# Kernel optimization log

Hardware: AMD Instinct MI355X
Metric: run time of the kernel (lower is better)

The kernel has to match this reference:

```python
import jax, jax.numpy as jnp
import numpy as np

B, T, N, DIN = 16, 40, 64, 64
H = 256          # n_hid == msg_out == gru_hid (required by the module's own shape constraints)
MSG_HID = 256
DOUT = 64
E = N * (N - 1)  # fully-connected directed graph, no self loops


def _linear_params(key, fin, fout):
    kw, kb = jax.random.split(key)
    s = 1.0 / np.sqrt(fin)
    w = jax.random.uniform(kw, (fout, fin), minval=-s, maxval=s, dtype=jnp.float32)
    b = jax.random.uniform(kb, (fout,), minval=-s, maxval=s, dtype=jnp.float32)
    return w, b


def setup_inputs() -> dict:
    key = jax.random.key(0)
    ks = jax.random.split(key, 16)
    # one-hot incidence matrices for all ordered node pairs (i != j)
    pairs = np.array([(i, j) for i in range(N) for j in range(N) if i != j])
    eye = np.eye(N, dtype=np.float32)
    rel_send = jnp.asarray(eye[pairs[:, 0]])  # [E, N]
    rel_rec = jnp.asarray(eye[pairs[:, 1]])   # [E, N]

    inputs = jax.random.normal(ks[0], (B, T, N, DIN), dtype=jnp.float32)
    rel_types = jax.random.uniform(ks[1], (B, E, 2), dtype=jnp.float32)

    d = {"inputs": inputs, "rel_rec": rel_rec, "rel_send": rel_send, "rel_types": rel_types}
    names_dims = [
        ("msg_fc1", 2 * H, MSG_HID), ("msg_fc2", MSG_HID, H),
        ("gru_ir", DIN, H), ("gru_hr", H, H),
        ("gru_ii", DIN, H), ("gru_hi", H, H),
        ("gru_in", DIN, H), ("gru_hn", H, H),
        ("out_fc1", H, H), ("out_fc2", H, H), ("out_fc3", H, DOUT),
    ]
    for k, (name, fin, fout) in zip(ks[2:13], names_dims):
        w, b = _linear_params(k, fin, fout)
        d[name + "_w"] = w
        d[name + "_b"] = b
    return d


def _lin(x, w, b):
    return x @ w.T + b


def reference(inputs, rel_rec, rel_send, rel_types,
              msg_fc1_w, msg_fc1_b, msg_fc2_w, msg_fc2_b,
              gru_ir_w, gru_ir_b, gru_hr_w, gru_hr_b,
              gru_ii_w, gru_ii_b, gru_hi_w, gru_hi_b,
              gru_in_w, gru_in_b, gru_hn_w, gru_hn_b,
              out_fc1_w, out_fc1_b, out_fc2_w, out_fc2_b, out_fc3_w, out_fc3_b):
    b, t, n, _ = inputs.shape
    # both edge-type branches share the same message MLP, so the summed
    # message equals msg * (rel_types[...,0] + rel_types[...,1])
    type_sum = rel_types[:, :, 0:1] + rel_types[:, :, 1:2]  # [B, E, 1]

    def step(hidden, xt):
        # node2edge on hidden: [B, E, 2H]
        senders = jnp.einsum('en,bnh->beh', rel_send, hidden)
        receivers = jnp.einsum('en,bnh->beh', rel_rec, hidden)
        pre_msg = jnp.concatenate([senders, receivers], axis=-1)
        msg = jax.nn.relu(_lin(pre_msg, msg_fc1_w, msg_fc1_b))
        msg = jax.nn.relu(_lin(msg, msg_fc2_w, msg_fc2_b))
        all_msgs = msg * type_sum                                   # [B, E, H]
        agg_msgs = jnp.einsum('beh,en->bnh', all_msgs, rel_rec)     # edge2node
        r = jax.nn.sigmoid(_lin(xt, gru_ir_w, gru_ir_b) + _lin(agg_msgs, gru_hr_w, gru_hr_b))
        i = jax.nn.sigmoid(_lin(xt, gru_ii_w, gru_ii_b) + _lin(agg_msgs, gru_hi_w, gru_hi_b))
        nn_ = jnp.tanh(_lin(xt, gru_in_w, gru_in_b) + r * _lin(agg_msgs, gru_hn_w, gru_hn_b))
        hidden = (1.0 - i) * nn_ + i * hidden
        pred = jax.nn.relu(_lin(hidden, out_fc1_w, out_fc1_b))
        pred = jax.nn.relu(_lin(pred, out_fc2_w, out_fc2_b))
        pred = _lin(pred, out_fc3_w, out_fc3_b)
        return hidden, pred

    xs = jnp.transpose(inputs[:, :-1], (1, 0, 2, 3))  # time-major [T-1, B, N, DIN]
    h0 = jnp.zeros((b, n, H), dtype=inputs.dtype)
    _, preds = jax.lax.scan(step, h0, xs)
    return jnp.transpose(preds, (1, 0, 2, 3))          # [B, T-1, N, n_out]
```

## Files before the change

### kernel.cpp

```cpp
#include <hip/hip_runtime.h>
#include <math.h>


namespace {
constexpr int kB = 16, kT = 40, kTS = 39, kN = 64, kDin = 64, kH = 256;
constexpr int kE = kN * (kN - 1);
constexpr int kBN = kB * kN;
constexpr int kDout = 64;
}

typedef _Float16 half8 __attribute__((ext_vector_type(8)));
typedef float f32x4 __attribute__((ext_vector_type(4)));

__device__ __forceinline__ float sigm(float x) { return 1.f / (1.f + expf(-x)); }

__device__ __forceinline__ unsigned short f2h(float x) {
    _Float16 h = (_Float16)x;
    return __builtin_bit_cast(unsigned short, h);
}

__device__ __forceinline__ uint4 pack8h(const float* x) {
    unsigned us[8];
    #pragma unroll
    for (int q = 0; q < 8; ++q) us[q] = f2h(x[q]);
    uint4 p;
    p.x = us[0] | (us[1] << 16); p.y = us[2] | (us[3] << 16);
    p.z = us[4] | (us[5] << 16); p.w = us[6] | (us[7] << 16);
    return p;
}

__global__ void setup_kernel(
    const float* __restrict__ rel_rec, const float* __restrict__ rel_send,
    const float* __restrict__ rel_types, const float* __restrict__ W2,
    const float* __restrict__ Whr, const float* __restrict__ Whi,
    const float* __restrict__ Whn, const float* __restrict__ Wir,
    const float* __restrict__ Wii, const float* __restrict__ Win,
    const float* __restrict__ W1,
    const float* __restrict__ bir, const float* __restrict__ bhr,
    const float* __restrict__ bii, const float* __restrict__ bhi,
    const float* __restrict__ fc1w, const float* __restrict__ fc2w,
    const float* __restrict__ fc3w,
    int* __restrict__ edge_at, float* __restrict__ ts,
    unsigned short* __restrict__ W2f,
    unsigned short* __restrict__ Wri,
    unsigned short* __restrict__ Wnh,
    unsigned short* __restrict__ Wnx,
    unsigned short* __restrict__ Wuv,
    unsigned short* __restrict__ F1, unsigned short* __restrict__ F2,
    unsigned short* __restrict__ F3,
    float* __restrict__ bri) {
    int idx = blockIdx.x * 256 + threadIdx.x;
    if (idx < kE) {
        int si = 0, ri = 0;
        for (int n = 0; n < kN; ++n) {
            if (rel_send[idx * kN + n] > 0.5f) si = n;
            if (rel_rec[idx * kN + n] > 0.5f) ri = n;
        }
        edge_at[ri * kN + si] = idx;
    }
    if (idx < kB * kE) ts[idx] = rel_types[2 * idx] + rel_types[2 * idx + 1];
    if (idx < kH * kH) {
        W2f[idx] = f2h(W2[idx]);
        Wnh[idx] = f2h(Whn[idx]);
        F1[idx] = f2h(fc1w[idx]);
        F2[idx] = f2h(fc2w[idx]);
    }
    if (idx < 512 * 320) {
        int row = idx / 320, k = idx - row * 320;
        float v;
        if (row < 256) v = (k < kH) ? Whr[row * kH + k] : Wir[row * kDin + k - kH];
        else { int o = row - 256; v = (k < kH) ? Whi[o * kH + k] : Wii[o * kDin + k - kH]; }
        Wri[idx] = f2h(v);
    }
    if (idx < kH * kDin) Wnx[idx] = f2h(Win[idx]);
    if (idx < 512 * 256) {
        int row = idx >> 8, k = idx & 255;
        float v = (row < 256) ? W1[row * 512 + k] : W1[(row - 256) * 512 + 256 + k];
        Wuv[idx] = f2h(v);
    }
    if (idx < kDout * kH) F3[idx] = f2h(fc3w[idx]);
    if (idx < 256) bri[idx] = bir[idx] + bhr[idx];
    else if (idx < 512) bri[idx] = bii[idx - 256] + bhi[idx - 256];
}

__global__ __launch_bounds__(512, 1)
void step_kernel(const float* __restrict__ hprev,
                 const float* __restrict__ inputs, int t,
                 const float* __restrict__ Uin, const float* __restrict__ Vin,
                 const unsigned short* __restrict__ W2f,
                 const float* __restrict__ b1, const float* __restrict__ b2,
                 const float* __restrict__ ts, const int* __restrict__ edge_at,
                 const unsigned short* __restrict__ Wri,
                 const unsigned short* __restrict__ Wnh,
                 const unsigned short* __restrict__ Wnx,
                 const unsigned short* __restrict__ Wuv,
                 const float* __restrict__ bri, const float* __restrict__ bhn,
                 const float* __restrict__ bin_,
                 float* __restrict__ hnew,
                 float* __restrict__ Uo, float* __restrict__ Vo) {
    __shared__ __align__(16) unsigned short h1[kN * kH];
    __shared__ float vjb4[4][kH];
    __shared__ float tss4[4][kN];
    __shared__ float aggL[4][kH];
    __shared__ __align__(16) unsigned short Zf[16 * 320];
    __shared__ __align__(16) unsigned short Hf[16 * 256];

    const int tid = threadIdx.x;
    const int lane = tid & 63, w = tid >> 6;
    const int mrow = lane & 15, mq = lane >> 4;
    const int cb = ((blockIdx.x & 7) << 5) | (blockIdx.x >> 3);
    const int m0 = cb * 4;
    const int b = cb >> 4, j0 = (cb & 15) * 4;

    {
        const int jj = tid >> 7, o = tid & 127;
        const int j = j0 + jj;
        vjb4[jj][o] = Vin[(size_t)(b * kN + j) * kH + o] + b1[o];
        vjb4[jj][o + 128] = Vin[(size_t)(b * kN + j) * kH + o + 128] + b1[o + 128];
        if (o < kN) {
            int e = edge_at[j * kN + o];
            tss4[jj][o] = (e < 0) ? 0.f : ts[b * kE + e];
        }
    }

    const int uo = tid & 31, ui0 = tid >> 5;
    float ur[4][8];
    #pragma unroll
    for (int p = 0; p < 4; ++p) {
        const float4* up = (const float4*)(Uin + (size_t)(b * kN + ui0 + 16 * p) * kH + uo * 8);
        *(float4*)&ur[p][0] = up[0];
        *(float4*)&ur[p][4] = up[1];
    }

    const unsigned short* Wp = W2f + (size_t)(w * 32 + mrow) * kH + mq * 8;
    half8 bb[8][2];
    #pragma unroll
    for (int kt = 0; kt < 8; ++kt)
        #pragma unroll
        for (int nf = 0; nf < 2; ++nf)
            bb[kt][nf] = *(const half8*)(Wp + nf * 16 * kH + kt * 32);
    __builtin_amdgcn_sched_barrier(0);
    __syncthreads();

    #pragma unroll 1
    for (int jj = 0; jj < 4; ++jj) {
        const int j = j0 + jj;
        {
            const int k0 = uo * 8;
            float vj[8];
            *(float4*)&vj[0] = *(const float4*)&vjb4[jj][k0];
            *(float4*)&vj[4] = *(const float4*)&vjb4[jj][k0 + 4];
            #pragma unroll
            for (int p = 0; p < 4; ++p) {
                const int i = ui0 + 16 * p;
                float x[8];
                #pragma unroll
                for (int q = 0; q < 8; ++q)
                    x[q] = (i == j) ? 0.f : fmaxf(ur[p][q] + vj[q], 0.f);
                const int byte = i * 512 + ((k0 * 2) ^ ((i & 7) << 4));
                *(uint4*)((char*)h1 + byte) = pack8h(x);
            }
        }
        __syncthreads();

        f32x4 acc[4][2];
        #pragma unroll
        for (int mf = 0; mf < 4; ++mf)
            #pragma unroll
            for (int nf = 0; nf < 2; ++nf) acc[mf][nf] = (f32x4){0.f, 0.f, 0.f, 0.f};
        #pragma unroll
        for (int kt = 0; kt < 8; ++kt) {
            const int k0 = kt * 32;
            half8 a[4];
            #pragma unroll
            for (int mf = 0; mf < 4; ++mf) {
                const int r = mf * 16 + mrow;
                const int byte = r * 512 + (((k0 + mq * 8) * 2) ^ ((r & 7) << 4));
                a[mf] = *(const half8*)((const char*)h1 + byte);
            }
            #pragma unroll
            for (int mf = 0; mf < 4; ++mf)
                #pragma unroll
                for (int nf = 0; nf < 2; ++nf)
                    acc[mf][nf] = __builtin_amdgcn_mfma_f32_16x16x32_f16(
                        a[mf], bb[kt][nf], acc[mf][nf], 0, 0, 0);
        }

        float tsr[16];
        #pragma unroll
        for (int mf = 0; mf < 4; ++mf)
            #pragma unroll
            for (int r = 0; r < 4; ++r)
                tsr[mf * 4 + r] = tss4[jj][mf * 16 + mq * 4 + r];
        #pragma unroll
        for (int nf = 0; nf < 2; ++nf) {
            const int col = w * 32 + nf * 16 + mrow;
            const float bv = b2[col];
            float s = 0.f;
            #pragma unroll
            for (int mf = 0; mf < 4; ++mf)
                #pragma unroll
                for (int r = 0; r < 4; ++r)
                    s += tsr[mf * 4 + r] * fmaxf(acc[mf][nf][r] + bv, 0.f);
            s += __shfl_xor(s, 16);
            s += __shfl_xor(s, 32);
            if (lane < 16) aggL[jj][col] = s;
        }
        __syncthreads();
    }

    {
        const uint4 z4 = {0u, 0u, 0u, 0u};
        for (int c = tid; c < 4 * 40; c += 512) {
            const int r = c / 40, g = c - r * 40;
            float x[8];
            if (g < 32) {
                #pragma unroll
                for (int q = 0; q < 8; ++q) x[q] = aggL[r][g * 8 + q];
            } else {
                const int grow = m0 + r, bb_ = grow >> 6, n = grow & 63;
                const float* xp = inputs + ((size_t)(bb_ * kT + t) * kN + n) * kDin + (g - 32) * 8;
                *(float4*)&x[0] = ((const float4*)xp)[0];
                *(float4*)&x[4] = ((const float4*)xp)[1];
            }
            const int byte = r * 640 + ((g ^ (r & 7)) << 4);
            *(uint4*)((char*)Zf + byte) = pack8h(x);
        }
        for (int c = tid; c < 12 * 40; c += 512) {
            const int r = 4 + c / 40, g = c - (c / 40) * 40;
            const int byte = r * 640 + ((g ^ (r & 7)) << 4);
            *(uint4*)((char*)Zf + byte) = z4;
        }
        for (int c = tid; c < 12 * 32; c += 512) {
            const int r = 4 + c / 32, g = c & 31;
            const int byte = r * 512 + ((g ^ (r & 7)) << 4);
            *(uint4*)((char*)Hf + byte) = z4;
        }
    }
    __syncthreads();

    #pragma unroll
    for (int nf = 0; nf < 2; ++nf) {
        const int col = w * 32 + nf * 16 + mrow;
        const unsigned short* WR = Wri + (size_t)col * 320 + mq * 8;
        const unsigned short* WI = Wri + (size_t)(256 + col) * 320 + mq * 8;
        const unsigned short* WNh = Wnh + (size_t)col * kH + mq * 8;
        const unsigned short* WNx = Wnx + (size_t)col * kDin + mq * 8;

        half8 rwa[10][3];
        #pragma unroll
        for (int kt = 0; kt < 10; ++kt) {
            rwa[kt][0] = *(const half8*)(WR + kt * 32);
            rwa[kt][1] = *(const half8*)(WI + kt * 32);
            if (kt < 8) rwa[kt][2] = *(const half8*)(WNh + kt * 32);
            else        rwa[kt][2] = *(const half8*)(WNx + (kt * 32 - 256));
        }
        __builtin_amdgcn_sched_barrier(0);

        f32x4 aR = {0.f,0.f,0.f,0.f}, aI = {0.f,0.f,0.f,0.f};
        f32x4 aNH = {0.f,0.f,0.f,0.f}, aNX = {0.f,0.f,0.f,0.f};
        #pragma unroll
        for (int kt = 0; kt < 10; ++kt) {
            const int g = kt * 4 + mq;
            const int byte = mrow * 640 + ((g ^ (mrow & 7)) << 4);
            half8 zf = *(const half8*)((const char*)Zf + byte);
            aR = __builtin_amdgcn_mfma_f32_16x16x32_f16(zf, rwa[kt][0], aR, 0, 0, 0);
            aI = __builtin_amdgcn_mfma_f32_16x16x32_f16(zf, rwa[kt][1], aI, 0, 0, 0);
            if (kt < 8) aNH = __builtin_amdgcn_mfma_f32_16x16x32_f16(zf, rwa[kt][2], aNH, 0, 0, 0);
            else        aNX = __builtin_amdgcn_mfma_f32_16x16x32_f16(zf, rwa[kt][2], aNX, 0, 0, 0);
        }

        if (mq == 0) {
            const float brv = bri[col], biv = bri[256 + col];
            const float bhnv = bhn[col], binv = bin_[col];
            #pragma unroll
            for (int reg = 0; reg < 4; ++reg) {
                const int lr = reg;
                const int grow = m0 + lr;
                float rg = sigm(aR[reg] + brv);
                float ig = sigm(aI[reg] + biv);
                float ng = tanhf(aNX[reg] + binv + rg * (aNH[reg] + bhnv));
                float h2 = (1.f - ig) * ng + ig * hprev[(size_t)grow * kH + col];
                hnew[(size_t)grow * kH + col] = h2;
                const int byte = lr * 512 + (((col >> 3) ^ (lr & 7)) << 4) + (col & 7) * 2;
                *(unsigned short*)((char*)Hf + byte) = f2h(h2);
            }
        }
    }
    __syncthreads();

    #pragma unroll
    for (int nf = 0; nf < 4; ++nf) {
        const int col = w * 64 + nf * 16 + mrow;
        const unsigned short* Wp2 = Wuv + (size_t)col * kH + mq * 8;
        half8 rwa[8];
        #pragma unroll
        for (int kt = 0; kt < 8; ++kt) rwa[kt] = *(const half8*)(Wp2 + kt * 32);
        __builtin_amdgcn_sched_barrier(0);
        f32x4 aUV = {0.f, 0.f, 0.f, 0.f};
        #pragma unroll
        for (int kt = 0; kt < 8; ++kt) {
            const int g = kt * 4 + mq;
            const int byte = mrow * 512 + ((g ^ (mrow & 7)) << 4);
            half8 zf = *(const half8*)((const char*)Hf + byte);
            aUV = __builtin_amdgcn_mfma_f32_16x16x32_f16(zf, rwa[kt], aUV, 0, 0, 0);
        }
        if (mq == 0) {
            #pragma unroll
            for (int reg = 0; reg < 4; ++reg) {
                const int grow = m0 + reg;
                const float v = aUV[reg];
                if (col < 256) Uo[(size_t)grow * kH + col] = v;
                else Vo[(size_t)grow * kH + col - 256] = v;
            }
        }
    }
}

__global__ __launch_bounds__(256, 2)
void out_kernel(const float* __restrict__ hist,
                const unsigned short* __restrict__ F1,
                const unsigned short* __restrict__ F2,
                const unsigned short* __restrict__ F3,
                const float* __restrict__ fc1b, const float* __restrict__ fc2b,
                const float* __restrict__ fc3b, float* __restrict__ out) {
    __shared__ __align__(16) unsigned short Af[64 * 256];
    __shared__ __align__(16) unsigned short Bf[64 * 256];
    const int m0 = blockIdx.x * 64;
    const int tid = threadIdx.x;
    const int lane = tid & 63, w = tid >> 6;
    const int mrow = lane & 15, mq = lane >> 4;

    #pragma unroll
    for (int it = 0; it < 8; ++it) {
        const int c = tid + it * 256;
        const int r = c >> 5, o = c & 31;
        const float* ap = hist + (size_t)(m0 + r) * kH + o * 8;
        float x[8];
        *(float4*)&x[0] = ((const float4*)ap)[0];
        *(float4*)&x[4] = ((const float4*)ap)[1];
        const int byte = r * 512 + ((o << 4) ^ ((r & 7) << 4));
        *(uint4*)((char*)Af + byte) = pack8h(x);
    }
    __syncthreads();

    #define LAYER(SRC, WW, BIAS, DST)                                           \
    {                                                                           \
        const unsigned short* wb = WW + (size_t)(w * 64 + mrow) * kH + mq * 8;  \
        half8 wall[8][4];                                                       \
        _Pragma("unroll")                                                       \
        for (int kt = 0; kt < 8; ++kt)                                          \
            _Pragma("unroll")                                                   \
            for (int nf = 0; nf < 4; ++nf)                                      \
                wall[kt][nf] = *(const half8*)(wb + nf * 16 * kH + kt * 32);    \
        __builtin_amdgcn_sched_barrier(0);                                      \
        f32x4 acc[4][4];                                                        \
        _Pragma("unroll")                                                       \
        for (int m = 0; m < 4; ++m)                                             \
            _Pragma("unroll")                                                   \
            for (int nf = 0; nf < 4; ++nf) acc[m][nf] = (f32x4){0.f,0.f,0.f,0.f};\
        _Pragma("unroll")                                                       \
        for (int kt = 0; kt < 8; ++kt) {                                        \
            const int k0 = kt * 32;                                             \
            half8 zf[4];                                                        \
            _Pragma("unroll")                                                   \
            for (int m = 0; m < 4; ++m) {                                       \
                const int r = m * 16 + mrow;                                    \
                const int byte = r * 512 + (((k0 + mq * 8) * 2) ^ ((r & 7) << 4)); \
                zf[m] = *(const half8*)((const char*)SRC + byte);               \
            }                                                                   \
            _Pragma("unroll")                                                   \
            for (int m = 0; m < 4; ++m)                                         \
                _Pragma("unroll")                                               \
                for (int nf = 0; nf < 4; ++nf)                                  \
                    acc[m][nf] = __builtin_amdgcn_mfma_f32_16x16x32_f16(        \
                        zf[m], wall[kt][nf], acc[m][nf], 0, 0, 0);              \
        }                                                                       \
        _Pragma("unroll")                                                       \
        for (int m = 0; m < 4; ++m)                                             \
            _Pragma("unroll")                                                   \
            for (int nf = 0; nf < 4; ++nf) {                                    \
                const int col = w * 64 + nf * 16 + mrow;                        \
                const float bv = BIAS[col];                                     \
                _Pragma("unroll")                                               \
                for (int reg = 0; reg < 4; ++reg) {                             \
                    const int lr = m * 16 + mq * 4 + reg;                       \
                    float v = fmaxf(acc[m][nf][reg] + bv, 0.f);                 \
                    const int byte = lr * 512 + (((col >> 3) ^ (lr & 7)) << 4) + (col & 7) * 2; \
                    *(unsigned short*)((char*)DST + byte) = f2h(v);             \
                }                                                               \
            }                                                                   \
        __syncthreads();                                                        \
    }

    LAYER(Af, F1, fc1b, Bf)
    LAYER(Bf, F2, fc2b, Af)

    {
        const int row = w * 16 + mrow;
        const unsigned short* wb = F3 + (size_t)row * kH + mq * 8;
        half8 wall[8];
        #pragma unroll
        for (int kt = 0; kt < 8; ++kt) wall[kt] = *(const half8*)(wb + kt * 32);
        __builtin_amdgcn_sched_barrier(0);
        f32x4 acc[4];
        #pragma unroll
        for (int m = 0; m < 4; ++m) acc[m] = (f32x4){0.f, 0.f, 0.f, 0.f};
        #pragma unroll
        for (int kt = 0; kt < 8; ++kt) {
            const int k0 = kt * 32;
            half8 zf[4];
            #pragma unroll
            for (int m = 0; m < 4; ++m) {
                const int r = m * 16 + mrow;
                const int byte = r * 512 + (((k0 + mq * 8) * 2) ^ ((r & 7) << 4));
                zf[m] = *(const half8*)((const char*)Af + byte);
            }
            #pragma unroll
            for (int m = 0; m < 4; ++m)
                acc[m] = __builtin_amdgcn_mfma_f32_16x16x32_f16(zf[m], wall[kt], acc[m], 0, 0, 0);
        }
        const int col = w * 16 + mrow;
        const float bv = fc3b[col];
        #pragma unroll
        for (int m = 0; m < 4; ++m)
            #pragma unroll
            for (int reg = 0; reg < 4; ++reg) {
                const int grow = m0 + m * 16 + mq * 4 + reg;
                const int t = grow >> 10, bn = grow & 1023, b = bn >> 6, n = bn & 63;
                out[(((size_t)b * kTS + t) * kN + n) * kDout + col] = acc[m][reg] + bv;
            }
    }
    #undef LAYER
}

extern "C" void kernel_launch(void* const* d_in, const int* in_sizes, int n_in,
                              void* d_out, int out_size, void* d_ws, size_t ws_size,
                              hipStream_t stream) {
    const float* inputs    = (const float*)d_in[0];
    const float* rel_rec   = (const float*)d_in[1];
    const float* rel_send  = (const float*)d_in[2];
    const float* rel_types = (const float*)d_in[3];
    const float* W1  = (const float*)d_in[4];  const float* b1  = (const float*)d_in[5];
    const float* W2  = (const float*)d_in[6];  const float* b2  = (const float*)d_in[7];
    const float* Wir = (const float*)d_in[8];  const float* bir = (const float*)d_in[9];
    const float* Whr = (const float*)d_in[10]; const float* bhr = (const float*)d_in[11];
    const float* Wii = (const float*)d_in[12]; const float* bii = (const float*)d_in[13];
    const float* Whi = (const float*)d_in[14]; const float* bhi = (const float*)d_in[15];
    const float* Win = (const float*)d_in[16]; const float* bin_ = (const float*)d_in[17];
    const float* Whn = (const float*)d_in[18]; const float* bhn = (const float*)d_in[19];
    const float* fc1w = (const float*)d_in[20]; const float* fc1b = (const float*)d_in[21];
    const float* fc2w = (const float*)d_in[22]; const float* fc2b = (const float*)d_in[23];
    const float* fc3w = (const float*)d_in[24]; const float* fc3b = (const float*)d_in[25];
    float* out = (float*)d_out;

    char* w = (char*)d_ws;
    auto take = [&](size_t bytes) { char* p = w; w += (bytes + 255) & ~(size_t)255; return p; };
    int* edge_at = (int*)take(kN * kN * 4);
    float* ts = (float*)take(kB * kE * 4);
    unsigned short* W2f = (unsigned short*)take(kH * kH * 2);
    unsigned short* Wri = (unsigned short*)take(512 * 320 * 2);
    unsigned short* Wnh = (unsigned short*)take(kH * kH * 2);
    unsigned short* Wnx = (unsigned short*)take(kH * kDin * 2);
    unsigned short* Wuv = (unsigned short*)take(512 * 256 * 2);
    unsigned short* F1 = (unsigned short*)take(kH * kH * 2);
    unsigned short* F2 = (unsigned short*)take(kH * kH * 2);
    unsigned short* F3 = (unsigned short*)take(kDout * kH * 2);
    float* bri = (float*)take(512 * 4);
    float* Ua = (float*)take((size_t)kBN * kH * 4);
    float* Va = (float*)take((size_t)kBN * kH * 4);
    float* Ub = (float*)take((size_t)kBN * kH * 4);
    float* Vb = (float*)take((size_t)kBN * kH * 4);
    float* hh = (float*)w;

    hipMemsetAsync(edge_at, 0xFF, kN * kN * 4, stream);
    setup_kernel<<<640, 256, 0, stream>>>(
        rel_rec, rel_send, rel_types, W2, Whr, Whi, Whn, Wir, Wii, Win, W1,
        bir, bhr, bii, bhi, fc1w, fc2w, fc3w,
        edge_at, ts, W2f, Wri, Wnh, Wnx, Wuv, F1, F2, F3, bri);
    hipMemsetAsync(Ua, 0, (size_t)kBN * kH * 4, stream);
    hipMemsetAsync(Va, 0, (size_t)kBN * kH * 4, stream);
    hipMemsetAsync(hh, 0, (size_t)kBN * kH * 4, stream);

    float* Uc = Ua; float* Vc = Va; float* Un = Ub; float* Vn = Vb;
    for (int t = 0; t < kTS; ++t) {
        step_kernel<<<kBN / 4, 512, 0, stream>>>(
            hh + (size_t)t * kBN * kH, inputs, t, Uc, Vc,
            W2f, b1, b2, ts, edge_at, Wri, Wnh, Wnx, Wuv, bri, bhn, bin_,
            hh + (size_t)(t + 1) * kBN * kH, Un, Vn);
        float* tmp;
        tmp = Uc; Uc = Un; Un = tmp;
        tmp = Vc; Vc = Vn; Vn = tmp;
    }
    out_kernel<<<kTS * kBN / 64, 256, 0, stream>>>(
        hh + (size_t)kBN * kH, F1, F2, F3, fc1b, fc2b, fc3b, out);
}
```

Measured before the change: 1.560 ms.

## Fuse all timesteps into one persistent kernel with per-batch grid barriers

Replaces the 39 per-timestep launches with a single persistent kernel of 256 blocks. Each block loops over time and synchronises only with the 16 blocks of its batch through an atomic counter barrier. The hidden state is kept in registers instead of reread from global memory, and the zero-padding of the shared tiles is done once. This removes launch overhead and the global inter-step dependency, at the cost of spin-wait barriers and the requirement that all 256 blocks be co-resident, which a 256-CU device at one block per CU can satisfy.

```diff
diff --git a/kernel.cpp b/kernel.cpp
--- a/kernel.cpp
+++ b/kernel.cpp
@@ -84,20 +84,20 @@
 }
 
 __global__ __launch_bounds__(512, 1)
-void step_kernel(const float* __restrict__ hprev,
-                 const float* __restrict__ inputs, int t,
-                 const float* __restrict__ Uin, const float* __restrict__ Vin,
-                 const unsigned short* __restrict__ W2f,
-                 const float* __restrict__ b1, const float* __restrict__ b2,
-                 const float* __restrict__ ts, const int* __restrict__ edge_at,
-                 const unsigned short* __restrict__ Wri,
-                 const unsigned short* __restrict__ Wnh,
-                 const unsigned short* __restrict__ Wnx,
-                 const unsigned short* __restrict__ Wuv,
-                 const float* __restrict__ bri, const float* __restrict__ bhn,
-                 const float* __restrict__ bin_,
-                 float* __restrict__ hnew,
-                 float* __restrict__ Uo, float* __restrict__ Vo) {
+void step_all_kernel(const float* __restrict__ inputs,
+                     float* __restrict__ Ua, float* __restrict__ Va,
+                     float* __restrict__ Ub, float* __restrict__ Vb,
+                     const unsigned short* __restrict__ W2f,
+                     const float* __restrict__ b1, const float* __restrict__ b2,
+                     const float* __restrict__ ts, const int* __restrict__ edge_at,
+                     const unsigned short* __restrict__ Wri,
+                     const unsigned short* __restrict__ Wnh,
+                     const unsigned short* __restrict__ Wnx,
+                     const unsigned short* __restrict__ Wuv,
+                     const float* __restrict__ bri, const float* __restrict__ bhn,
+                     const float* __restrict__ bin_,
+                     float* __restrict__ hh,
+                     unsigned int* __restrict__ bar) {
     __shared__ __align__(16) unsigned short h1[kN * kH];
     __shared__ float vjb4[4][kH];
     __shared__ float tss4[4][kN];
@@ -111,27 +111,15 @@
     const int cb = ((blockIdx.x & 7) << 5) | (blockIdx.x >> 3);
     const int m0 = cb * 4;
     const int b = cb >> 4, j0 = (cb & 15) * 4;
+    const int grp = b;
 
     {
         const int jj = tid >> 7, o = tid & 127;
-        const int j = j0 + jj;
-        vjb4[jj][o] = Vin[(size_t)(b * kN + j) * kH + o] + b1[o];
-        vjb4[jj][o + 128] = Vin[(size_t)(b * kN + j) * kH + o + 128] + b1[o + 128];
         if (o < kN) {
-            int e = edge_at[j * kN + o];
+            int e = edge_at[(j0 + jj) * kN + o];
             tss4[jj][o] = (e < 0) ? 0.f : ts[b * kE + e];
         }
     }
-
-    const int uo = tid & 31, ui0 = tid >> 5;
-    float ur[4][8];
-    #pragma unroll
-    for (int p = 0; p < 4; ++p) {
-        const float4* up = (const float4*)(Uin + (size_t)(b * kN + ui0 + 16 * p) * kH + uo * 8);
-        *(float4*)&ur[p][0] = up[0];
-        *(float4*)&ur[p][4] = up[1];
-    }
-
     const unsigned short* Wp = W2f + (size_t)(w * 32 + mrow) * kH + mq * 8;
     half8 bb[8][2];
     #pragma unroll
@@ -140,77 +128,111 @@
         for (int nf = 0; nf < 2; ++nf)
             bb[kt][nf] = *(const half8*)(Wp + nf * 16 * kH + kt * 32);
     __builtin_amdgcn_sched_barrier(0);
-    __syncthreads();
-
-    #pragma unroll 1
-    for (int jj = 0; jj < 4; ++jj) {
-        const int j = j0 + jj;
-        {
-            const int k0 = uo * 8;
-            float vj[8];
-            *(float4*)&vj[0] = *(const float4*)&vjb4[jj][k0];
-            *(float4*)&vj[4] = *(const float4*)&vjb4[jj][k0 + 4];
-            #pragma unroll
-            for (int p = 0; p < 4; ++p) {
-                const int i = ui0 + 16 * p;
-                float x[8];
-                #pragma unroll
-                for (int q = 0; q < 8; ++q)
-                    x[q] = (i == j) ? 0.f : fmaxf(ur[p][q] + vj[q], 0.f);
-                const int byte = i * 512 + ((k0 * 2) ^ ((i & 7) << 4));
-                *(uint4*)((char*)h1 + byte) = pack8h(x);
-            }
-        }
-        __syncthreads();
-
-        f32x4 acc[4][2];
-        #pragma unroll
-        for (int mf = 0; mf < 4; ++mf)
-            #pragma unroll
-            for (int nf = 0; nf < 2; ++nf) acc[mf][nf] = (f32x4){0.f, 0.f, 0.f, 0.f};
-        #pragma unroll
-        for (int kt = 0; kt < 8; ++kt) {
-            const int k0 = kt * 32;
-            half8 a[4];
-            #pragma unroll
-            for (int mf = 0; mf < 4; ++mf) {
-                const int r = mf * 16 + mrow;
-                const int byte = r * 512 + (((k0 + mq * 8) * 2) ^ ((r & 7) << 4));
-                a[mf] = *(const half8*)((const char*)h1 + byte);
-            }
-            #pragma unroll
-            for (int mf = 0; mf < 4; ++mf)
-                #pragma unroll
-                for (int nf = 0; nf < 2; ++nf)
-                    acc[mf][nf] = __builtin_amdgcn_mfma_f32_16x16x32_f16(
-                        a[mf], bb[kt][nf], acc[mf][nf], 0, 0, 0);
-        }
-
-        float tsr[16];
-        #pragma unroll
-        for (int mf = 0; mf < 4; ++mf)
-            #pragma unroll
-            for (int r = 0; r < 4; ++r)
-                tsr[mf * 4 + r] = tss4[jj][mf * 16 + mq * 4 + r];
-        #pragma unroll
-        for (int nf = 0; nf < 2; ++nf) {
-            const int col = w * 32 + nf * 16 + mrow;
-            const float bv = b2[col];
-            float s = 0.f;
-            #pragma unroll
-            for (int mf = 0; mf < 4; ++mf)
-                #pragma unroll
-                for (int r = 0; r < 4; ++r)
-                    s += tsr[mf * 4 + r] * fmaxf(acc[mf][nf][r] + bv, 0.f);
-            s += __shfl_xor(s, 16);
-            s += __shfl_xor(s, 32);
-            if (lane < 16) aggL[jj][col] = s;
-        }
-        __syncthreads();
-    }
-
     {
         const uint4 z4 = {0u, 0u, 0u, 0u};
+        for (int c = tid; c < 12 * 40; c += 512) {
+            const int r = 4 + c / 40, g = c - (c / 40) * 40;
+            *(uint4*)((char*)Zf + r * 640 + ((g ^ (r & 7)) << 4)) = z4;
+        }
+        for (int c = tid; c < 12 * 32; c += 512) {
+            const int r = 4 + c / 32, g = c & 31;
+            *(uint4*)((char*)Hf + r * 512 + ((g ^ (r & 7)) << 4)) = z4;
+        }
+    }
+
+    const int uo = tid & 31, ui0 = tid >> 5;
+    float hreg[2][4];
+    #pragma unroll
+    for (int nf = 0; nf < 2; ++nf)
+        #pragma unroll
+        for (int r = 0; r < 4; ++r) hreg[nf][r] = 0.f;
+
+    const float* Uc = Ua; const float* Vc = Va;
+    float* Un = Ub; float* Vn = Vb;
+
+    #pragma unroll 1
+    for (int t = 0; t < kTS; ++t) {
+        {
+            const int jj = tid >> 7, o = tid & 127;
+            const int j = j0 + jj;
+            vjb4[jj][o] = Vc[(size_t)(b * kN + j) * kH + o] + b1[o];
+            vjb4[jj][o + 128] = Vc[(size_t)(b * kN + j) * kH + o + 128] + b1[o + 128];
+        }
+        float ur[4][8];
+        #pragma unroll
+        for (int p = 0; p < 4; ++p) {
+            const float4* up = (const float4*)(Uc + (size_t)(b * kN + ui0 + 16 * p) * kH + uo * 8);
+            *(float4*)&ur[p][0] = up[0];
+            *(float4*)&ur[p][4] = up[1];
+        }
+        __syncthreads();
+
+        #pragma unroll 1
+        for (int jj = 0; jj < 4; ++jj) {
+            const int j = j0 + jj;
+            {
+                const int k0 = uo * 8;
+                float vj[8];
+                *(float4*)&vj[0] = *(const float4*)&vjb4[jj][k0];
+                *(float4*)&vj[4] = *(const float4*)&vjb4[jj][k0 + 4];
+                #pragma unroll
+                for (int p = 0; p < 4; ++p) {
+                    const int i = ui0 + 16 * p;
+                    float x[8];
+                    #pragma unroll
+                    for (int q = 0; q < 8; ++q)
+                        x[q] = (i == j) ? 0.f : fmaxf(ur[p][q] + vj[q], 0.f);
+                    *(uint4*)((char*)h1 + i * 512 + ((k0 * 2) ^ ((i & 7) << 4))) = pack8h(x);
+                }
+            }
+            __syncthreads();
+
+            f32x4 acc[4][2];
+            #pragma unroll
+            for (int mf = 0; mf < 4; ++mf)
+                #pragma unroll
+                for (int nf = 0; nf < 2; ++nf) acc[mf][nf] = (f32x4){0.f, 0.f, 0.f, 0.f};
+            #pragma unroll
+            for (int kt = 0; kt < 8; ++kt) {
+                const int k0 = kt * 32;
+                half8 a[4];
+                #pragma unroll
+                for (int mf = 0; mf < 4; ++mf) {
+                    const int r = mf * 16 + mrow;
+                    a[mf] = *(const half8*)((const char*)h1 + r * 512 +
+                                            (((k0 + mq * 8) * 2) ^ ((r & 7) << 4)));
+                }
+                #pragma unroll
+                for (int mf = 0; mf < 4; ++mf)
+                    #pragma unroll
+                    for (int nf = 0; nf < 2; ++nf)
+                        acc[mf][nf] = __builtin_amdgcn_mfma_f32_16x16x32_f16(
+                            a[mf], bb[kt][nf], acc[mf][nf], 0, 0, 0);
+            }
+
+            float tsr[16];
+            #pragma unroll
+            for (int mf = 0; mf < 4; ++mf)
+                #pragma unroll
+                for (int r = 0; r < 4; ++r)
+                    tsr[mf * 4 + r] = tss4[jj][mf * 16 + mq * 4 + r];
+            #pragma unroll
+            for (int nf = 0; nf < 2; ++nf) {
+                const int col = w * 32 + nf * 16 + mrow;
+                const float bv = b2[col];
+                float s = 0.f;
+                #pragma unroll
+                for (int mf = 0; mf < 4; ++mf)
+                    #pragma unroll
+                    for (int r = 0; r < 4; ++r)
+                        s += tsr[mf * 4 + r] * fmaxf(acc[mf][nf][r] + bv, 0.f);
+                s += __shfl_xor(s, 16);
+                s += __shfl_xor(s, 32);
+                if (lane < 16) aggL[jj][col] = s;
+            }
+            __syncthreads();
+        }
+
         for (int c = tid; c < 4 * 40; c += 512) {
             const int r = c / 40, g = c - r * 40;
             float x[8];
@@ -223,96 +245,101 @@
                 *(float4*)&x[0] = ((const float4*)xp)[0];
                 *(float4*)&x[4] = ((const float4*)xp)[1];
             }
-            const int byte = r * 640 + ((g ^ (r & 7)) << 4);
-            *(uint4*)((char*)Zf + byte) = pack8h(x);
-        }
-        for (int c = tid; c < 12 * 40; c += 512) {
-            const int r = 4 + c / 40, g = c - (c / 40) * 40;
-            const int byte = r * 640 + ((g ^ (r & 7)) << 4);
-            *(uint4*)((char*)Zf + byte) = z4;
-        }
-        for (int c = tid; c < 12 * 32; c += 512) {
-            const int r = 4 + c / 32, g = c & 31;
-            const int byte = r * 512 + ((g ^ (r & 7)) << 4);
-            *(uint4*)((char*)Hf + byte) = z4;
-        }
-    }
-    __syncthreads();
-
-    #pragma unroll
-    for (int nf = 0; nf < 2; ++nf) {
-        const int col = w * 32 + nf * 16 + mrow;
-        const unsigned short* WR = Wri + (size_t)col * 320 + mq * 8;
-        const unsigned short* WI = Wri + (size_t)(256 + col) * 320 + mq * 8;
-        const unsigned short* WNh = Wnh + (size_t)col * kH + mq * 8;
-        const unsigned short* WNx = Wnx + (size_t)col * kDin + mq * 8;
-
-        half8 rwa[10][3];
-        #pragma unroll
-        for (int kt = 0; kt < 10; ++kt) {
-            rwa[kt][0] = *(const half8*)(WR + kt * 32);
-            rwa[kt][1] = *(const half8*)(WI + kt * 32);
-            if (kt < 8) rwa[kt][2] = *(const half8*)(WNh + kt * 32);
-            else        rwa[kt][2] = *(const half8*)(WNx + (kt * 32 - 256));
-        }
-        __builtin_amdgcn_sched_barrier(0);
-
-        f32x4 aR = {0.f,0.f,0.f,0.f}, aI = {0.f,0.f,0.f,0.f};
-        f32x4 aNH = {0.f,0.f,0.f,0.f}, aNX = {0.f,0.f,0.f,0.f};
-        #pragma unroll
-        for (int kt = 0; kt < 10; ++kt) {
-            const int g = kt * 4 + mq;
-            const int byte = mrow * 640 + ((g ^ (mrow & 7)) << 4);
-            half8 zf = *(const half8*)((const char*)Zf + byte);
-            aR = __builtin_amdgcn_mfma_f32_16x16x32_f16(zf, rwa[kt][0], aR, 0, 0, 0);
-            aI = __builtin_amdgcn_mfma_f32_16x16x32_f16(zf, rwa[kt][1], aI, 0, 0, 0);
-            if (kt < 8) aNH = __builtin_amdgcn_mfma_f32_16x16x32_f16(zf, rwa[kt][2], aNH, 0, 0, 0);
-            else        aNX = __builtin_amdgcn_mfma_f32_16x16x32_f16(zf, rwa[kt][2], aNX, 0, 0, 0);
-        }
-
-        if (mq == 0) {
-            const float brv = bri[col], biv = bri[256 + col];
-            const float bhnv = bhn[col], binv = bin_[col];
-            #pragma unroll
-            for (int reg = 0; reg < 4; ++reg) {
-                const int lr = reg;
-                const int grow = m0 + lr;
-                float rg = sigm(aR[reg] + brv);
-                float ig = sigm(aI[reg] + biv);
-                float ng = tanhf(aNX[reg] + binv + rg * (aNH[reg] + bhnv));
-                float h2 = (1.f - ig) * ng + ig * hprev[(size_t)grow * kH + col];
-                hnew[(size_t)grow * kH + col] = h2;
-                const int byte = lr * 512 + (((col >> 3) ^ (lr & 7)) << 4) + (col & 7) * 2;
-                *(unsigned short*)((char*)Hf + byte) = f2h(h2);
-            }
-        }
-    }
-    __syncthreads();
-
-    #pragma unroll
-    for (int nf = 0; nf < 4; ++nf) {
-        const int col = w * 64 + nf * 16 + mrow;
-        const unsigned short* Wp2 = Wuv + (size_t)col * kH + mq * 8;
-        half8 rwa[8];
-        #pragma unroll
-        for (int kt = 0; kt < 8; ++kt) rwa[kt] = *(const half8*)(Wp2 + kt * 32);
-        __builtin_amdgcn_sched_barrier(0);
-        f32x4 aUV = {0.f, 0.f, 0.f, 0.f};
-        #pragma unroll
-        for (int kt = 0; kt < 8; ++kt) {
-            const int g = kt * 4 + mq;
-            const int byte = mrow * 512 + ((g ^ (mrow & 7)) << 4);
-            half8 zf = *(const half8*)((const char*)Hf + byte);
-            aUV = __builtin_amdgcn_mfma_f32_16x16x32_f16(zf, rwa[kt], aUV, 0, 0, 0);
-        }
-        if (mq == 0) {
-            #pragma unroll
-            for (int reg = 0; reg < 4; ++reg) {
-                const int grow = m0 + reg;
-                const float v = aUV[reg];
-                if (col < 256) Uo[(size_t)grow * kH + col] = v;
-                else Vo[(size_t)grow * kH + col - 256] = v;
-            }
+            *(uint4*)((char*)Zf + r * 640 + ((g ^ (r & 7)) << 4)) = pack8h(x);
+        }
+        __syncthreads();
+
+        #pragma unroll
+        for (int nf = 0; nf < 2; ++nf) {
+            const int col = w * 32 + nf * 16 + mrow;
+            const unsigned short* WR = Wri + (size_t)col * 320 + mq * 8;
+            const unsigned short* WI = Wri + (size_t)(256 + col) * 320 + mq * 8;
+            const unsigned short* WNh = Wnh + (size_t)col * kH + mq * 8;
+            const unsigned short* WNx = Wnx + (size_t)col * kDin + mq * 8;
+
+            half8 rwa[10][3];
+            #pragma unroll
+            for (int kt = 0; kt < 10; ++kt) {
+                rwa[kt][0] = *(const half8*)(WR + kt * 32);
+                rwa[kt][1] = *(const half8*)(WI + kt * 32);
+                if (kt < 8) rwa[kt][2] = *(const half8*)(WNh + kt * 32);
+                else        rwa[kt][2] = *(const half8*)(WNx + (kt * 32 - 256));
+            }
+            __builtin_amdgcn_sched_barrier(0);
+
+            f32x4 aR = {0.f,0.f,0.f,0.f}, aI = {0.f,0.f,0.f,0.f};
+            f32x4 aNH = {0.f,0.f,0.f,0.f}, aNX = {0.f,0.f,0.f,0.f};
+            #pragma unroll
+            for (int kt = 0; kt < 10; ++kt) {
+                const int g = kt * 4 + mq;
+                half8 zf = *(const half8*)((const char*)Zf + mrow * 640 + ((g ^ (mrow & 7)) << 4));
+                aR = __builtin_amdgcn_mfma_f32_16x16x32_f16(zf, rwa[kt][0], aR, 0, 0, 0);
+                aI = __builtin_amdgcn_mfma_f32_16x16x32_f16(zf, rwa[kt][1], aI, 0, 0, 0);
+                if (kt < 8) aNH = __builtin_amdgcn_mfma_f32_16x16x32_f16(zf, rwa[kt][2], aNH, 0, 0, 0);
+                else        aNX = __builtin_amdgcn_mfma_f32_16x16x32_f16(zf, rwa[kt][2], aNX, 0, 0, 0);
+            }
+
+            if (mq == 0) {
+                const float brv = bri[col], biv = bri[256 + col];
+                const float bhnv = bhn[col], binv = bin_[col];
+                #pragma unroll
+                for (int reg = 0; reg < 4; ++reg) {
+                    const int grow = m0 + reg;
+                    float rg = sigm(aR[reg] + brv);
+                    float ig = sigm(aI[reg] + biv);
+                    float ng = tanhf(aNX[reg] + binv + rg * (aNH[reg] + bhnv));
+                    float h2 = (1.f - ig) * ng + ig * hreg[nf][reg];
+                    hreg[nf][reg] = h2;
+                    hh[((size_t)(t + 1) * kBN + grow) * kH + col] = h2;
+                    *(unsigned short*)((char*)Hf + reg * 512 +
+                        (((col >> 3) ^ (reg & 7)) << 4) + (col & 7) * 2) = f2h(h2);
+                }
+            }
+        }
+        __syncthreads();
+
+        #pragma unroll
+        for (int nf = 0; nf < 4; ++nf) {
+            const int col = w * 64 + nf * 16 + mrow;
+            const unsigned short* Wp2 = Wuv + (size_t)col * kH + mq * 8;
+            half8 rwa[8];
+            #pragma unroll
+            for (int kt = 0; kt < 8; ++kt) rwa[kt] = *(const half8*)(Wp2 + kt * 32);
+            __builtin_amdgcn_sched_barrier(0);
+            f32x4 aUV = {0.f, 0.f, 0.f, 0.f};
+            #pragma unroll
+            for (int kt = 0; kt < 8; ++kt) {
+                const int g = kt * 4 + mq;
+                half8 zf = *(const half8*)((const char*)Hf + mrow * 512 + ((g ^ (mrow & 7)) << 4));
+                aUV = __builtin_amdgcn_mfma_f32_16x16x32_f16(zf, rwa[kt], aUV, 0, 0, 0);
+            }
+            if (mq == 0) {
+                #pragma unroll
+                for (int reg = 0; reg < 4; ++reg) {
+                    const int grow = m0 + reg;
+                    const float v = aUV[reg];
+                    if (col < 256) Un[(size_t)grow * kH + col] = v;
+                    else Vn[(size_t)grow * kH + col - 256] = v;
+                }
+            }
+        }
+
+        if (t + 1 < kTS) {
+            __threadfence();
+            __syncthreads();
+            if (tid == 0)
+                __hip_atomic_fetch_add(&bar[grp], 1u, __ATOMIC_RELEASE,
+                                       __HIP_MEMORY_SCOPE_AGENT);
+            const unsigned target = 16u * (unsigned)(t + 1);
+            if (tid == 0) {
+                while (__hip_atomic_load(&bar[grp], __ATOMIC_ACQUIRE,
+                                         __HIP_MEMORY_SCOPE_AGENT) < target)
+                    __builtin_amdgcn_s_sleep(2);
+            }
+            __syncthreads();
+            __threadfence();
+            const float* tU = Uc; Uc = Un; Un = (float*)tU;
+            const float* tV = Vc; Vc = Vn; Vn = (float*)tV;
         }
     }
 }
@@ -467,6 +494,7 @@
     unsigned short* F2 = (unsigned short*)take(kH * kH * 2);
     unsigned short* F3 = (unsigned short*)take(kDout * kH * 2);
     float* bri = (float*)take(512 * 4);
+    unsigned int* bar = (unsigned int*)take(kB * 4);
     float* Ua = (float*)take((size_t)kBN * kH * 4);
     float* Va = (float*)take((size_t)kBN * kH * 4);
     float* Ub = (float*)take((size_t)kBN * kH * 4);
@@ -474,24 +502,18 @@
     float* hh = (float*)w;
 
     hipMemsetAsync(edge_at, 0xFF, kN * kN * 4, stream);
+    hipMemsetAsync(bar, 0, kB * 4, stream);
     setup_kernel<<<640, 256, 0, stream>>>(
         rel_rec, rel_send, rel_types, W2, Whr, Whi, Whn, Wir, Wii, Win, W1,
         bir, bhr, bii, bhi, fc1w, fc2w, fc3w,
         edge_at, ts, W2f, Wri, Wnh, Wnx, Wuv, F1, F2, F3, bri);
     hipMemsetAsync(Ua, 0, (size_t)kBN * kH * 4, stream);
     hipMemsetAsync(Va, 0, (size_t)kBN * kH * 4, stream);
-    hipMemsetAsync(hh, 0, (size_t)kBN * kH * 4, stream);
-
-    float* Uc = Ua; float* Vc = Va; float* Un = Ub; float* Vn = Vb;
-    for (int t = 0; t < kTS; ++t) {
-        step_kernel<<<kBN / 4, 512, 0, stream>>>(
-            hh + (size_t)t * kBN * kH, inputs, t, Uc, Vc,
-            W2f, b1, b2, ts, edge_at, Wri, Wnh, Wnx, Wuv, bri, bhn, bin_,
-            hh + (size_t)(t + 1) * kBN * kH, Un, Vn);
-        float* tmp;
-        tmp = Uc; Uc = Un; Un = tmp;
-        tmp = Vc; Vc = Vn; Vn = tmp;
-    }
+
+    step_all_kernel<<<256, 512, 0, stream>>>(
+        inputs, Ua, Va, Ub, Vb, W2f, b1, b2, ts, edge_at,
+        Wri, Wnh, Wnx, Wuv, bri, bhn, bin_, hh, bar);
+
     out_kernel<<<kTS * kBN / 64, 256, 0, stream>>>(
         hh + (size_t)kBN * kH, F1, F2, F3, fc1b, fc2b, fc3b, out);
 }
```

Result: slower. 5.044 ms (+223.3%).
